# Optimization experiments

Hardware: AMD Instinct MI355X
Metric: run time of the kernel (lower is better)

## Reference

```python
import jax, jax.numpy as jnp
import numpy as np

N_NODES = 50000
N_EDGES = 800000
D_IN = 128
D_OUT = 128
LN_EPS = 1e-5


def setup_inputs() -> dict:
    key = jax.random.key(0)
    ks = jax.random.split(key, 8)
    h = jax.random.normal(ks[0], (N_NODES, D_IN), dtype=jnp.float32)
    edge_row = jax.random.randint(ks[1], (N_EDGES,), 0, N_NODES, dtype=jnp.int32)
    edge_col = jax.random.randint(ks[2], (N_EDGES,), 0, N_NODES, dtype=jnp.int32)
    # normalized-ish edge weights (e.g. 1/deg values in GraphSAGE-mean)
    edge_val = jax.random.uniform(ks[3], (N_EDGES,), dtype=jnp.float32) / 16.0
    scale = 1.0 / np.sqrt(D_IN)
    W_self = jax.random.normal(ks[4], (D_OUT, D_IN), dtype=jnp.float32) * scale
    b_self = jnp.zeros((D_OUT,), dtype=jnp.float32)
    W_neigh = jax.random.normal(ks[5], (D_OUT, D_IN), dtype=jnp.float32) * scale
    b_neigh = jnp.zeros((D_OUT,), dtype=jnp.float32)
    ln_gamma = jnp.ones((2 * D_OUT,), dtype=jnp.float32)
    ln_beta = jnp.zeros((2 * D_OUT,), dtype=jnp.float32)
    return {"h": h, "edge_row": edge_row, "edge_col": edge_col, "edge_val": edge_val,
            "W_self": W_self, "b_self": b_self, "W_neigh": W_neigh, "b_neigh": b_neigh,
            "ln_gamma": ln_gamma, "ln_beta": ln_beta}


def reference(h, edge_row, edge_col, edge_val, W_self, b_self, W_neigh, b_neigh, ln_gamma, ln_beta):
    out_nodes = N_NODES  # adj.sizes()[0]
    # support = adj.spmm(h): gather source features, scale by edge value, scatter-add to dest rows
    msgs = h[edge_col] * edge_val[:, None]                      # [E, D_IN]
    support = jax.ops.segment_sum(msgs, edge_row, num_segments=out_nodes)  # [N, D_IN]
    self_h = h[:out_nodes] @ W_self.T + b_self                  # [N, D_OUT]
    neigh_h = support @ W_neigh.T + b_neigh                     # [N, D_OUT]
    x = jnp.concatenate([self_h, neigh_h], axis=1)              # [N, 2*D_OUT]
    x = jax.nn.relu(x)
    # LayerNorm over last dim, elementwise affine
    mu = jnp.mean(x, axis=-1, keepdims=True)
    var = jnp.mean(jnp.square(x - mu), axis=-1, keepdims=True)
    x = (x - mu) * jax.lax.rsqrt(var + LN_EPS)
    return x * ln_gamma + ln_beta
```

## Files before the change

### kernel.cpp

```cpp
#include <hip/hip_runtime.h>
#include <hip/hip_fp16.h>
#include <cstddef>

#define DIN 128
#define BROWS 128
#define EPB 8192
#define MAXB 512
#define PCAP 3072

typedef short bf16x8 __attribute__((ext_vector_type(8)));
typedef float f32x4  __attribute__((ext_vector_type(4)));

__device__ inline unsigned short f2bf(float x) {
    union { float f; unsigned u; } v; v.f = x;
    unsigned r = v.u + 0x7FFFu + ((v.u >> 16) & 1u);
    return (unsigned short)(r >> 16);
}
__device__ inline float bf_lo(unsigned x) { return __int_as_float(x << 16); }
__device__ inline float bf_hi(unsigned x) { return __int_as_float(x & 0xFFFF0000u); }


__global__ __launch_bounds__(256) void prep_kernel(
    const float* __restrict__ h, const int* __restrict__ erow,
    int* __restrict__ ghist, unsigned short* __restrict__ hb,
    int n_conv, int n_edges, int nbkt, int nhb)
{
    __shared__ int hist[MAXB];
    int t = threadIdx.x;
    int bid = blockIdx.x;

    if (bid < nhb) {
        for (int i = t; i < nbkt; i += 256) hist[i] = 0;
        __syncthreads();
        int s = bid * EPB;
        int e = s + EPB; if (e > n_edges) e = n_edges;
        for (int i = s + t; i < e; i += 256)
            atomicAdd(&hist[erow[i] >> 7], 1);
        __syncthreads();
        for (int i = t; i < nbkt; i += 256)
            if (hist[i] > 0) atomicAdd(&ghist[i], hist[i]);
    }

    int i = bid * 256 + t;
    if (i < n_conv) {
        const float4* p = (const float4*)(h + (size_t)i * 8);
        float4 a = p[0], b = p[1];
        bf16x8 v;
        v[0] = f2bf(a.x); v[1] = f2bf(a.y); v[2] = f2bf(a.z); v[3] = f2bf(a.w);
        v[4] = f2bf(b.x); v[5] = f2bf(b.y); v[6] = f2bf(b.z); v[7] = f2bf(b.w);
        *(bf16x8*)(hb + (size_t)i * 8) = v;
    }
}

__global__ __launch_bounds__(256) void bucket_scan(
    const int* __restrict__ ghist, int* __restrict__ bbase,
    int* __restrict__ ccur, int nbkt, int n_edges)
{
    __shared__ int cnt[MAXB];
    __shared__ int s[256];
    int t = threadIdx.x;
    for (int b = t; b < MAXB; b += 256)
        cnt[b] = (b < nbkt) ? ghist[b] : 0;
    __syncthreads();
    int pair = cnt[2 * t] + cnt[2 * t + 1];
    int x = pair;
    s[t] = x;
    __syncthreads();
    for (int off = 1; off < 256; off <<= 1) {
        int y = (t >= off) ? s[t - off] : 0;
        __syncthreads();
        x += y;
        s[t] = x;
        __syncthreads();
    }
    int excl = x - pair;
    if (2 * t < nbkt)     { bbase[2 * t] = excl;              ccur[2 * t] = excl; }
    if (2 * t + 1 < nbkt) { bbase[2 * t + 1] = excl + cnt[2 * t];
                            ccur[2 * t + 1] = excl + cnt[2 * t]; }
    if (t == 255) bbase[nbkt] = n_edges;
}

__global__ __launch_bounds__(256) void bin_coarse(
    const int* __restrict__ erow, const int* __restrict__ ecol,
    const float* __restrict__ evalv, int* __restrict__ ccur,
    int2* __restrict__ recs, int n_edges, int nbkt)
{
    __shared__ int hist[MAXB];
    __shared__ int wbase[MAXB];
    __shared__ int cur[MAXB];
    int t = threadIdx.x;
    for (int i = t; i < nbkt; i += 256) { hist[i] = 0; cur[i] = 0; }
    int start = blockIdx.x * EPB;
    int end = start + EPB; if (end > n_edges) end = n_edges;
    int myrows[EPB / 256];
    int cnt = 0;
    __syncthreads();
    for (int e = start + t; e < end; e += 256) {
        int r = erow[e];
        myrows[cnt++] = r;
        atomicAdd(&hist[r >> 7], 1);
    }
    __syncthreads();
    for (int b = t; b < nbkt; b += 256)
        if (hist[b] > 0) wbase[b] = atomicAdd(&ccur[b], hist[b]);
    __syncthreads();
    cnt = 0;
    for (int e = start + t; e < end; e += 256) {
        int r = myrows[cnt++];
        int b = r >> 7;
        int off = atomicAdd(&cur[b], 1);
        unsigned short vb = __half_as_ushort(__float2half_rn(evalv[e]));
        int2 rec;
        rec.x = r & (BROWS - 1);
        rec.y = (int)((unsigned)(ecol[e] & 0xFFFF) | ((unsigned)vb << 16));
        recs[wbase[b] + off] = rec;
    }
}

__global__ __launch_bounds__(1024) void row_gather(
    const int2* __restrict__ recs, const int* __restrict__ bbase,
    const unsigned short* __restrict__ hb, unsigned short* __restrict__ support,
    int n_nodes)
{
    __shared__ unsigned plist[PCAP];
    __shared__ int cnt[BROWS];
    __shared__ int lbase[BROWS];
    __shared__ int cur[BROWS];

    int t = threadIdx.x;
    int b = blockIdx.x;
    int start = bbase[b];
    int end = bbase[b + 1];

    if (t < BROWS) { cnt[t] = 0; cur[t] = 0; }
    __syncthreads();

    for (int i = start + t; i < end; i += 1024)
        atomicAdd(&cnt[recs[i].x], 1);
    __syncthreads();

    if (t < BROWS) lbase[t] = cnt[t];
    __syncthreads();
    for (int off = 1; off < BROWS; off <<= 1) {
        int v = (t < BROWS && t >= off) ? lbase[t - off] : 0;
        __syncthreads();
        if (t < BROWS) lbase[t] += v;
        __syncthreads();
    }
    if (t < BROWS) lbase[t] -= cnt[t];
    __syncthreads();

    for (int i = start + t; i < end; i += 1024) {
        int2 rec = recs[i];
        int pos = lbase[rec.x] + atomicAdd(&cur[rec.x], 1);
        if (pos < PCAP) plist[pos] = (unsigned)rec.y;
    }
    __syncthreads();

    int wave = t >> 6;
    int lane = t & 63;
    const unsigned* hu = (const unsigned*)hb;

#pragma unroll
    for (int rr = 0; rr < 8; rr++) {
        int r = wave * 8 + rr;
        int s = lbase[r];
        int e2 = s + cnt[r];

        float ax[8], ay[8];
#pragma unroll
        for (int k = 0; k < 8; k++) { ax[k] = 0.f; ay[k] = 0.f; }

        int e = s;
        for (; e + 7 < e2; e += 8) {
            unsigned p[8];
#pragma unroll
            for (int k = 0; k < 8; k++) p[k] = plist[e + k];
            unsigned x[8];
#pragma unroll
            for (int k = 0; k < 8; k++)
                x[k] = hu[(size_t)(p[k] & 0xFFFFu) * 64 + lane];
#pragma unroll
            for (int k = 0; k < 8; k++) {
                float v = __half2float(__ushort_as_half((unsigned short)(p[k] >> 16)));
                ax[k] += bf_lo(x[k]) * v;
                ay[k] += bf_hi(x[k]) * v;
            }
        }
        for (; e + 3 < e2; e += 4) {
            unsigned p[4];
#pragma unroll
            for (int k = 0; k < 4; k++) p[k] = plist[e + k];
            unsigned x[4];
#pragma unroll
            for (int k = 0; k < 4; k++)
                x[k] = hu[(size_t)(p[k] & 0xFFFFu) * 64 + lane];
#pragma unroll
            for (int k = 0; k < 4; k++) {
                float v = __half2float(__ushort_as_half((unsigned short)(p[k] >> 16)));
                ax[k] += bf_lo(x[k]) * v;
                ay[k] += bf_hi(x[k]) * v;
            }
        }
        for (; e < e2; e++) {
            unsigned p = plist[e];
            unsigned x = hu[(size_t)(p & 0xFFFFu) * 64 + lane];
            float v = __half2float(__ushort_as_half((unsigned short)(p >> 16)));
            ax[0] += bf_lo(x) * v; ay[0] += bf_hi(x) * v;
        }

        float sx = 0.f, sy = 0.f;
#pragma unroll
        for (int k = 0; k < 8; k++) { sx += ax[k]; sy += ay[k]; }

        int row = b * BROWS + r;
        if (row < n_nodes) {
            unsigned outp = (unsigned)f2bf(sx) | ((unsigned)f2bf(sy) << 16);
            ((unsigned*)support)[(size_t)row * 64 + lane] = outp;
        }
    }
}

__global__ __launch_bounds__(256) void mfma_gemm_ln(
    const unsigned short* __restrict__ hb,
    const unsigned short* __restrict__ support,
    const float* __restrict__ Ws, const float* __restrict__ bs,
    const float* __restrict__ Wn, const float* __restrict__ bn,
    const float* __restrict__ gamma, const float* __restrict__ beta,
    float* __restrict__ out,
    int n_nodes)
{
    __shared__ short Wlds[2][128][128];

    const int tid = threadIdx.x;

    {
        int d = tid >> 1;
        int half = tid & 1;
#pragma unroll
        for (int m = 0; m < 2; m++) {
            const float* row = (m ? Wn : Ws) + (size_t)d * 128;
#pragma unroll
            for (int c8 = 0; c8 < 8; c8++) {
                int ch = half * 8 + c8;
                const float4* p = (const float4*)(row + ch * 8);
                float4 x0 = p[0], x1 = p[1];
                bf16x8 v;
                v[0] = f2bf(x0.x); v[1] = f2bf(x0.y);
                v[2] = f2bf(x0.z); v[3] = f2bf(x0.w);
                v[4] = f2bf(x1.x); v[5] = f2bf(x1.y);
                v[6] = f2bf(x1.z); v[7] = f2bf(x1.w);
                int phys = ch ^ (d & 7);
                *(bf16x8*)&Wlds[m][d][phys * 8] = v;
            }
        }
    }
    __syncthreads();

    const int wave = tid >> 6;
    const int lane = tid & 63;
    const int q = lane >> 4;
    const int c = lane & 15;
    const int n0 = blockIdx.x * 64 + wave * 16;
    if (n0 >= n_nodes) return;

    f32x4 accS[8], accN[8];
#pragma unroll
    for (int t = 0; t < 8; t++) {
        accS[t] = (f32x4){0.f, 0.f, 0.f, 0.f};
        accN[t] = (f32x4){0.f, 0.f, 0.f, 0.f};
    }

    const bf16x8* ph = (const bf16x8*)(hb + (size_t)(n0 + c) * DIN + q * 8);
    const bf16x8* ps = (const bf16x8*)(support + (size_t)(n0 + c) * DIN + q * 8);

#pragma unroll
    for (int ks = 0; ks < 4; ks++) {
        bf16x8 aH = ph[ks * 4];
        bf16x8 aS = ps[ks * 4];
        int cl = ks * 4 + q;
#pragma unroll
        for (int t = 0; t < 8; t++) {
            int d = t * 16 + c;
            int phys = cl ^ (d & 7);
            bf16x8 bS = *(const bf16x8*)&Wlds[0][d][phys * 8];
            accS[t] = __builtin_amdgcn_mfma_f32_16x16x32_bf16(aH, bS, accS[t], 0, 0, 0);
            bf16x8 bN = *(const bf16x8*)&Wlds[1][d][phys * 8];
            accN[t] = __builtin_amdgcn_mfma_f32_16x16x32_bf16(aS, bN, accN[t], 0, 0, 0);
        }
    }

    float sum[4] = {0.f, 0.f, 0.f, 0.f};
    float ssq[4] = {0.f, 0.f, 0.f, 0.f};
#pragma unroll
    for (int t = 0; t < 8; t++) {
        float bS = bs[t * 16 + c];
        float bN = bn[t * 16 + c];
#pragma unroll
        for (int r = 0; r < 4; r++) {
            float v1 = accS[t][r] + bS; v1 = v1 > 0.f ? v1 : 0.f; accS[t][r] = v1;
            float v2 = accN[t][r] + bN; v2 = v2 > 0.f ? v2 : 0.f; accN[t][r] = v2;
            sum[r] += v1 + v2;
            ssq[r] += v1 * v1 + v2 * v2;
        }
    }
#pragma unroll
    for (int off = 8; off >= 1; off >>= 1) {
#pragma unroll
        for (int r = 0; r < 4; r++) {
            sum[r] += __shfl_xor(sum[r], off, 64);
            ssq[r] += __shfl_xor(ssq[r], off, 64);
        }
    }
    float mu[4], rstd[4];
#pragma unroll
    for (int r = 0; r < 4; r++) {
        mu[r] = sum[r] * (1.f / 256.f);
        float var = ssq[r] * (1.f / 256.f) - mu[r] * mu[r];
        rstd[r] = rsqrtf(var + 1e-5f);
    }

#pragma unroll
    for (int t = 0; t < 8; t++) {
        int dS = t * 16 + c;
        int dN = 128 + t * 16 + c;
        float gS = gamma[dS], btS = beta[dS];
        float gN = gamma[dN], btN = beta[dN];
#pragma unroll
        for (int r = 0; r < 4; r++) {
            size_t rowbase = (size_t)(n0 + q * 4 + r) * 256;
            out[rowbase + dS] = (accS[t][r] - mu[r]) * rstd[r] * gS + btS;
            out[rowbase + dN] = (accN[t][r] - mu[r]) * rstd[r] * gN + btN;
        }
    }
}

extern "C" void kernel_launch(void* const* d_in, const int* in_sizes, int n_in,
                              void* d_out, int out_size, void* d_ws, size_t ws_size,
                              hipStream_t stream)
{
    const float* h     = (const float*)d_in[0];
    const int*   erow  = (const int*)d_in[1];
    const int*   ecol  = (const int*)d_in[2];
    const float* evalv = (const float*)d_in[3];
    const float* Ws    = (const float*)d_in[4];
    const float* bs    = (const float*)d_in[5];
    const float* Wn    = (const float*)d_in[6];
    const float* bn    = (const float*)d_in[7];
    const float* gamma = (const float*)d_in[8];
    const float* beta  = (const float*)d_in[9];
    float* out = (float*)d_out;

    int n_nodes = in_sizes[0] / DIN;
    int n_edges = in_sizes[1];

    int nbkt = (n_nodes + BROWS - 1) / BROWS;
    int nhb  = (n_edges + EPB - 1) / EPB;

    char* ws = (char*)d_ws;
    unsigned short* hb      = (unsigned short*)ws;  ws += (size_t)n_nodes * DIN * sizeof(short);
    unsigned short* support = (unsigned short*)ws;  ws += (size_t)n_nodes * DIN * sizeof(short);
    int2* recs = (int2*)ws;                         ws += (size_t)n_edges * sizeof(int2);
    int* ghist = (int*)ws;                          ws += (size_t)nbkt * sizeof(int);
    int* bbase = (int*)ws;                          ws += (size_t)(nbkt + 1) * sizeof(int);
    int* ccur  = (int*)ws;                          ws += (size_t)nbkt * sizeof(int);

    int n_conv = n_nodes * DIN / 8;
    int pb = (n_conv + 255) / 256;
    if (pb < nhb) pb = nhb;

    hipMemsetAsync(ghist, 0, (size_t)nbkt * sizeof(int), stream);
    prep_kernel <<<pb,   256, 0, stream>>>(h, erow, ghist, hb, n_conv, n_edges, nbkt, nhb);
    bucket_scan <<<1,    256, 0, stream>>>(ghist, bbase, ccur, nbkt, n_edges);
    bin_coarse  <<<nhb,  256, 0, stream>>>(erow, ecol, evalv, ccur, recs, n_edges, nbkt);
    row_gather  <<<nbkt, 1024, 0, stream>>>(recs, bbase, hb, support, n_nodes);

    int gb = (n_nodes + 63) / 64;
    mfma_gemm_ln<<<gb, 256, 0, stream>>>(hb, support, Ws, bs, Wn, bn, gamma, beta,
                                         out, n_nodes);
}
```

Baseline: 200.5 us.

## Split row_gather buckets across two blocks and pre-convert weights to bf16 once

row_gather now launches two blocks per 128-row bucket, each handling 64 rows and filtering records by half, doubling block count for better CU occupancy while each block rescans the bucket's records. Weight fp32->bf16 conversion moves from every GEMM block into extra prep_kernel blocks writing a shared bf16 buffer, so each GEMM block just copies bf16 into LDS. Costs: duplicated record reads in row_gather and a smaller per-block edge capacity (PCAP2=2048) that could truncate dense rows.

```diff
diff --git a/kernel.cpp b/kernel.cpp
--- a/kernel.cpp
+++ b/kernel.cpp
@@ -4,9 +4,10 @@
 
 #define DIN 128
 #define BROWS 128
+#define HROWS 64
 #define EPB 8192
 #define MAXB 512
-#define PCAP 3072
+#define PCAP2 2048
 
 typedef short bf16x8 __attribute__((ext_vector_type(8)));
 typedef float f32x4  __attribute__((ext_vector_type(4)));
@@ -22,8 +23,10 @@
 
 __global__ __launch_bounds__(256) void prep_kernel(
     const float* __restrict__ h, const int* __restrict__ erow,
+    const float* __restrict__ Ws, const float* __restrict__ Wn,
     int* __restrict__ ghist, unsigned short* __restrict__ hb,
-    int n_conv, int n_edges, int nbkt, int nhb)
+    unsigned short* __restrict__ wbf,
+    int n_conv, int n_edges, int nbkt, int nhb, int pb)
 {
     __shared__ int hist[MAXB];
     int t = threadIdx.x;
@@ -41,14 +44,28 @@
             if (hist[i] > 0) atomicAdd(&ghist[i], hist[i]);
     }
 
-    int i = bid * 256 + t;
-    if (i < n_conv) {
-        const float4* p = (const float4*)(h + (size_t)i * 8);
-        float4 a = p[0], b = p[1];
-        bf16x8 v;
-        v[0] = f2bf(a.x); v[1] = f2bf(a.y); v[2] = f2bf(a.z); v[3] = f2bf(a.w);
-        v[4] = f2bf(b.x); v[5] = f2bf(b.y); v[6] = f2bf(b.z); v[7] = f2bf(b.w);
-        *(bf16x8*)(hb + (size_t)i * 8) = v;
+    if (bid < pb) {
+        int i = bid * 256 + t;
+        if (i < n_conv) {
+            const float4* p = (const float4*)(h + (size_t)i * 8);
+            float4 a = p[0], b = p[1];
+            bf16x8 v;
+            v[0] = f2bf(a.x); v[1] = f2bf(a.y); v[2] = f2bf(a.z); v[3] = f2bf(a.w);
+            v[4] = f2bf(b.x); v[5] = f2bf(b.y); v[6] = f2bf(b.z); v[7] = f2bf(b.w);
+            *(bf16x8*)(hb + (size_t)i * 8) = v;
+        }
+    } else {
+        int wi = (bid - pb) * 256 + t;
+        if (wi < 4096) {
+            const float* src = (wi < 2048) ? (Ws + (size_t)wi * 8)
+                                           : (Wn + (size_t)(wi - 2048) * 8);
+            const float4* p = (const float4*)src;
+            float4 a = p[0], b = p[1];
+            bf16x8 v;
+            v[0] = f2bf(a.x); v[1] = f2bf(a.y); v[2] = f2bf(a.z); v[3] = f2bf(a.w);
+            v[4] = f2bf(b.x); v[5] = f2bf(b.y); v[6] = f2bf(b.z); v[7] = f2bf(b.w);
+            *(bf16x8*)(wbf + (size_t)wi * 8) = v;
+        }
     }
 }
 
@@ -122,38 +139,44 @@
     const unsigned short* __restrict__ hb, unsigned short* __restrict__ support,
     int n_nodes)
 {
-    __shared__ unsigned plist[PCAP];
-    __shared__ int cnt[BROWS];
-    __shared__ int lbase[BROWS];
-    __shared__ int cur[BROWS];
+    __shared__ unsigned plist[PCAP2];
+    __shared__ int cnt[HROWS];
+    __shared__ int lbase[HROWS];
+    __shared__ int cur[HROWS];
 
     int t = threadIdx.x;
-    int b = blockIdx.x;
+    int b = blockIdx.x >> 1;
+    int rlo = (blockIdx.x & 1) * HROWS;
     int start = bbase[b];
     int end = bbase[b + 1];
 
-    if (t < BROWS) { cnt[t] = 0; cur[t] = 0; }
-    __syncthreads();
-
-    for (int i = start + t; i < end; i += 1024)
-        atomicAdd(&cnt[recs[i].x], 1);
-    __syncthreads();
-
-    if (t < BROWS) lbase[t] = cnt[t];
-    __syncthreads();
-    for (int off = 1; off < BROWS; off <<= 1) {
-        int v = (t < BROWS && t >= off) ? lbase[t - off] : 0;
-        __syncthreads();
-        if (t < BROWS) lbase[t] += v;
-        __syncthreads();
-    }
-    if (t < BROWS) lbase[t] -= cnt[t];
+    if (t < HROWS) { cnt[t] = 0; cur[t] = 0; }
+    __syncthreads();
+
+    for (int i = start + t; i < end; i += 1024) {
+        int r = recs[i].x - rlo;
+        if ((unsigned)r < (unsigned)HROWS) atomicAdd(&cnt[r], 1);
+    }
+    __syncthreads();
+
+    if (t < HROWS) lbase[t] = cnt[t];
+    __syncthreads();
+    for (int off = 1; off < HROWS; off <<= 1) {
+        int v = (t < HROWS && t >= off) ? lbase[t - off] : 0;
+        __syncthreads();
+        if (t < HROWS) lbase[t] += v;
+        __syncthreads();
+    }
+    if (t < HROWS) lbase[t] -= cnt[t];
     __syncthreads();
 
     for (int i = start + t; i < end; i += 1024) {
         int2 rec = recs[i];
-        int pos = lbase[rec.x] + atomicAdd(&cur[rec.x], 1);
-        if (pos < PCAP) plist[pos] = (unsigned)rec.y;
+        int r = rec.x - rlo;
+        if ((unsigned)r < (unsigned)HROWS) {
+            int pos = lbase[r] + atomicAdd(&cur[r], 1);
+            if (pos < PCAP2) plist[pos] = (unsigned)rec.y;
+        }
     }
     __syncthreads();
 
@@ -162,8 +185,8 @@
     const unsigned* hu = (const unsigned*)hb;
 
 #pragma unroll
-    for (int rr = 0; rr < 8; rr++) {
-        int r = wave * 8 + rr;
+    for (int rr = 0; rr < 4; rr++) {
+        int r = wave * 4 + rr;
         int s = lbase[r];
         int e2 = s + cnt[r];
 
@@ -213,7 +236,7 @@
 #pragma unroll
         for (int k = 0; k < 8; k++) { sx += ax[k]; sy += ay[k]; }
 
-        int row = b * BROWS + r;
+        int row = b * BROWS + rlo + r;
         if (row < n_nodes) {
             unsigned outp = (unsigned)f2bf(sx) | ((unsigned)f2bf(sy) << 16);
             ((unsigned*)support)[(size_t)row * 64 + lane] = outp;
@@ -224,8 +247,8 @@
 __global__ __launch_bounds__(256) void mfma_gemm_ln(
     const unsigned short* __restrict__ hb,
     const unsigned short* __restrict__ support,
-    const float* __restrict__ Ws, const float* __restrict__ bs,
-    const float* __restrict__ Wn, const float* __restrict__ bn,
+    const unsigned short* __restrict__ wbf,
+    const float* __restrict__ bs, const float* __restrict__ bn,
     const float* __restrict__ gamma, const float* __restrict__ beta,
     float* __restrict__ out,
     int n_nodes)
@@ -235,24 +258,15 @@
     const int tid = threadIdx.x;
 
     {
-        int d = tid >> 1;
-        int half = tid & 1;
-#pragma unroll
-        for (int m = 0; m < 2; m++) {
-            const float* row = (m ? Wn : Ws) + (size_t)d * 128;
-#pragma unroll
-            for (int c8 = 0; c8 < 8; c8++) {
-                int ch = half * 8 + c8;
-                const float4* p = (const float4*)(row + ch * 8);
-                float4 x0 = p[0], x1 = p[1];
-                bf16x8 v;
-                v[0] = f2bf(x0.x); v[1] = f2bf(x0.y);
-                v[2] = f2bf(x0.z); v[3] = f2bf(x0.w);
-                v[4] = f2bf(x1.x); v[5] = f2bf(x1.y);
-                v[6] = f2bf(x1.z); v[7] = f2bf(x1.w);
-                int phys = ch ^ (d & 7);
-                *(bf16x8*)&Wlds[m][d][phys * 8] = v;
-            }
+        const uint4* wsrc = (const uint4*)wbf;
+#pragma unroll
+        for (int j = 0; j < 16; j++) {
+            int i = j * 256 + tid;
+            int m = i >> 11;
+            int d = (i >> 4) & 127;
+            int ch = i & 15;
+            int phys = ch ^ (d & 7);
+            *(uint4*)&Wlds[m][d][phys * 8] = wsrc[i];
         }
     }
     __syncthreads();
@@ -361,6 +375,7 @@
     unsigned short* hb      = (unsigned short*)ws;  ws += (size_t)n_nodes * DIN * sizeof(short);
     unsigned short* support = (unsigned short*)ws;  ws += (size_t)n_nodes * DIN * sizeof(short);
     int2* recs = (int2*)ws;                         ws += (size_t)n_edges * sizeof(int2);
+    unsigned short* wbf = (unsigned short*)ws;      ws += (size_t)2 * 128 * 128 * sizeof(short);
     int* ghist = (int*)ws;                          ws += (size_t)nbkt * sizeof(int);
     int* bbase = (int*)ws;                          ws += (size_t)(nbkt + 1) * sizeof(int);
     int* ccur  = (int*)ws;                          ws += (size_t)nbkt * sizeof(int);
@@ -370,12 +385,13 @@
     if (pb < nhb) pb = nhb;
 
     hipMemsetAsync(ghist, 0, (size_t)nbkt * sizeof(int), stream);
-    prep_kernel <<<pb,   256, 0, stream>>>(h, erow, ghist, hb, n_conv, n_edges, nbkt, nhb);
+    prep_kernel <<<pb + 16, 256, 0, stream>>>(h, erow, Ws, Wn, ghist, hb, wbf,
+                                              n_conv, n_edges, nbkt, nhb, pb);
     bucket_scan <<<1,    256, 0, stream>>>(ghist, bbase, ccur, nbkt, n_edges);
     bin_coarse  <<<nhb,  256, 0, stream>>>(erow, ecol, evalv, ccur, recs, n_edges, nbkt);
-    row_gather  <<<nbkt, 1024, 0, stream>>>(recs, bbase, hb, support, n_nodes);
+    row_gather  <<<nbkt * 2, 1024, 0, stream>>>(recs, bbase, hb, support, n_nodes);
 
     int gb = (n_nodes + 63) / 64;
-    mfma_gemm_ln<<<gb, 256, 0, stream>>>(hb, support, Ws, bs, Wn, bn, gamma, beta,
+    mfma_gemm_ln<<<gb, 256, 0, stream>>>(hb, support, wbf, bs, bn, gamma, beta,
                                          out, n_nodes);
 }
```

After: 188.5 us. 1.06x faster.
